# Optimization experiments

Hardware: AMD Instinct MI355X
Metric: run time of the kernel (lower is better)

The kernel has to match this reference:

```python
import jax, jax.numpy as jnp
import numpy as np

EMBED_DIM = 2048
NUM_HEADS = 16
HEAD_DIM = EMBED_DIM // NUM_HEADS
SCALES = [(1, 1, 1), (1, 2, 2), (1, 4, 4), (1, 6, 6), (1, 8, 8),
          (1, 12, 12), (1, 16, 16), (1, 20, 20), (1, 24, 24), (1, 32, 32)]
LENS = [t * h * w for (t, h, w) in SCALES]
SEQ_LEN = int(np.sum(LENS))  # 2521
BATCH = 2
MAX_SCALE_MUL = float(np.log(100.0))


def _block_causal_bias():
    # VAR-style: queries in scale-block i attend to all keys up to end of block i.
    cum = np.cumsum(LENS)
    q_end = np.repeat(cum, LENS)                      # [L] visible kv length per query
    visible = np.arange(SEQ_LEN)[None, :] < q_end[:, None]
    bias = np.where(visible, 0.0, -np.inf).astype(np.float32)
    return jnp.asarray(bias)[None, None]              # [1,1,L,L]


def setup_inputs() -> dict:
    key = jax.random.key(0)
    ks = jax.random.split(key, 8)
    C, H, hd, L, B = EMBED_DIM, NUM_HEADS, HEAD_DIM, SEQ_LEN, BATCH
    x = jax.random.normal(ks[0], (B, L, C), dtype=jnp.float32)
    W_qkv = jax.random.normal(ks[1], (3 * C, C), dtype=jnp.float32) * (1.0 / np.sqrt(C))
    q_bias = jnp.zeros((C,), jnp.float32)
    v_bias = jnp.zeros((C,), jnp.float32)
    scale_mul_log = jnp.full((1, H, 1, 1), np.log(4.0), jnp.float32)
    proj_W = jax.random.normal(ks[2], (C, C), dtype=jnp.float32) * (1.0 / np.sqrt(C))
    proj_b = jnp.zeros((C,), jnp.float32)
    # 2D RoPE cache, pre-sliced for scale_ind=0: (2,1,1,1,L,hd//2) = (cos, sin)
    angles = jax.random.uniform(ks[3], (L, hd // 2), dtype=jnp.float32, maxval=2.0 * np.pi)
    rope_cache = jnp.stack([jnp.cos(angles), jnp.sin(angles)])[:, None, None, None]
    attn_bias = _block_causal_bias()
    return {"x": x, "W_qkv": W_qkv, "q_bias": q_bias, "v_bias": v_bias,
            "scale_mul_log": scale_mul_log, "proj_W": proj_W, "proj_b": proj_b,
            "rope_cache": rope_cache, "attn_bias": attn_bias}


def _l2norm(t, eps=1e-12):
    # torch F.normalize: x / max(||x||_2, eps)
    n = jnp.sqrt(jnp.sum(t * t, axis=-1, keepdims=True))
    return t / jnp.maximum(n, eps)


def reference(x, W_qkv, q_bias, v_bias, scale_mul_log, proj_W, proj_b, rope_cache, attn_bias):
    B, L, C = x.shape
    H, hd = NUM_HEADS, HEAD_DIM
    bias = jnp.concatenate([q_bias, jnp.zeros_like(q_bias), v_bias])
    qkv = x @ W_qkv.T + bias                               # [B,L,3C]
    qkv = qkv.reshape(B, L, 3, H, hd).transpose(2, 0, 3, 1, 4)  # [3,B,H,L,hd]
    q, k, v = qkv[0], qkv[1], qkv[2]
    # cosine attention: L2-norm q,k; q scaled by clamped learnable per-head scale
    scale_mul = jnp.exp(jnp.minimum(scale_mul_log, MAX_SCALE_MUL))
    q = _l2norm(q) * scale_mul
    k = _l2norm(k)
    # 2D RoPE applied jointly to q and k
    qk = jnp.stack([q, k]).reshape(2, B, H, L, hd // 2, 2)
    cos, sin = rope_cache[0], rope_cache[1]                # [1,1,1,L,hd//2]
    re = cos * qk[..., 0] - sin * qk[..., 1]
    im = sin * qk[..., 0] + cos * qk[..., 1]
    qk = jnp.stack([re, im], axis=-1).reshape(2, B, H, L, hd)
    q, k = qk[0], qk[1]
    # SDPA with scale=1 (cos_attn) and additive block-causal bias
    scores = jnp.einsum('bhqd,bhkd->bhqk', q, k) + attn_bias
    attn = jax.nn.softmax(scores, axis=-1)
    out = jnp.einsum('bhqk,bhkd->bhqd', attn, v)           # [B,H,L,hd]
    out = out.transpose(0, 2, 1, 3).reshape(B, L, C)
    return out @ proj_W.T + proj_b
```

## Files before the change

kernel.cpp:

```cpp
#include <hip/hip_runtime.h>
#include <stdint.h>

#define SEQL 2521
#define LPAD 2560
#define NB 2
#define NH 16
#define HD 128
#define CD 2048
#define KD 2048

typedef float f32x4 __attribute__((ext_vector_type(4)));
typedef __bf16 bf16x8 __attribute__((ext_vector_type(8)));
typedef unsigned short u16x8 __attribute__((ext_vector_type(8)));

static __device__ __forceinline__ unsigned short bf16r(float f){
  union { float f; unsigned u; } v; v.f = f;
  unsigned r = v.u + 0x7FFFu + ((v.u >> 16) & 1u);
  return (unsigned short)(r >> 16);
}
static __device__ __forceinline__ float bf2f(unsigned short s){
  union { unsigned u; float f; } v; v.u = ((unsigned)s) << 16; return v.f;
}
static __device__ __forceinline__ bf16x8 asbf(u16x8 v){ return __builtin_bit_cast(bf16x8, v); }

typedef const __attribute__((address_space(1))) unsigned int* gas1_t;
typedef __attribute__((address_space(3))) unsigned int* las3_t;
static __device__ __forceinline__ void glds16(const void* g, void* l){
  __builtin_amdgcn_global_load_lds((gas1_t)g, (las3_t)l, 16, 0, 0);
}

__global__ __launch_bounds__(256) void prep_kernel(
    const float* __restrict__ x, const float* __restrict__ wqkv, const float* __restrict__ projw,
    unsigned short* __restrict__ xb, unsigned short* __restrict__ wb, unsigned short* __restrict__ pw)
{
  const int NX = (NB*LPAD*CD)/4;
  const int NW = (3*CD*CD)/4;
  const int NPj = (CD*CD)/4;
  const int total = NX + NW + NPj;
  for (int v = blockIdx.x*256 + threadIdx.x; v < total; v += gridDim.x*256){
    if (v < NX){
      int e = v << 2;
      int row = e >> 11, col = e & 2047;
      int b = (row >= LPAD) ? 1 : 0;
      int l = row - b*LPAD;
      ushort4 o;
      if (l < SEQL){
        const float4 f = *(const float4*)(x + (((long)(b*SEQL + l)) << 11) + col);
        o.x = bf16r(f.x); o.y = bf16r(f.y); o.z = bf16r(f.z); o.w = bf16r(f.w);
      } else { o.x = 0; o.y = 0; o.z = 0; o.w = 0; }
      *(ushort4*)(xb + e) = o;
    } else if (v < NX + NW){
      long i = (long)(v - NX) << 2;
      const float4 f = *(const float4*)(wqkv + i);
      ushort4 o; o.x=bf16r(f.x); o.y=bf16r(f.y); o.z=bf16r(f.z); o.w=bf16r(f.w);
      *(ushort4*)(wb + i) = o;
    } else {
      long i = (long)(v - NX - NW) << 2;
      const float4 f = *(const float4*)(projw + i);
      ushort4 o; o.x=bf16r(f.x); o.y=bf16r(f.y); o.z=bf16r(f.z); o.w=bf16r(f.w);
      *(ushort4*)(pw + i) = o;
    }
  }
}

static __device__ __forceinline__ void gemm_core(
    const unsigned short* __restrict__ A, const unsigned short* __restrict__ Bm,
    unsigned short* As, unsigned short* Bs, int m0, int n0, f32x4 acc[4][4])
{
  const int tid = threadIdx.x;
  const int w = tid >> 6, lane = tid & 63;
  const int g = lane >> 4, lr = lane & 15;
  const int wm = w >> 1, wn = w & 1;
  const unsigned short* aS0 = A + (long)(m0 + (tid >> 2))*KD + ((tid & 3) << 3);
  const unsigned short* aS1 = aS0 + (long)64*KD;
  const unsigned short* bS0 = Bm + (long)(n0 + (tid >> 2))*KD + ((tid & 3) << 3);
  const unsigned short* bS1 = bS0 + (long)64*KD;
  unsigned short* aD0 = As + (w << 9);
  unsigned short* aD1 = As + 2048 + (w << 9);
  unsigned short* bD0 = Bs + (w << 9);
  unsigned short* bD1 = Bs + 2048 + (w << 9);
  const unsigned short* aRd = As + ((wm << 6) + lr)*32 + (g << 3);
  const unsigned short* bRd = Bs + ((wn << 6) + lr)*32 + (g << 3);
  for (int kt = 0; kt < KD/32; ++kt){
    __syncthreads();
    const int ko = kt << 5;
    glds16(aS0 + ko, aD0);
    glds16(aS1 + ko, aD1);
    glds16(bS0 + ko, bD0);
    glds16(bS1 + ko, bD1);
    __syncthreads();
    u16x8 af[4], bfr[4];
#pragma unroll
    for (int i = 0; i < 4; ++i) af[i]  = *(const u16x8*)(aRd + i*16*32);
#pragma unroll
    for (int j = 0; j < 4; ++j) bfr[j] = *(const u16x8*)(bRd + j*16*32);
#pragma unroll
    for (int i = 0; i < 4; ++i)
#pragma unroll
      for (int j = 0; j < 4; ++j)
        acc[i][j] = __builtin_amdgcn_mfma_f32_16x16x32_bf16(asbf(af[i]), asbf(bfr[j]), acc[i][j], 0, 0, 0);
  }
}

__global__ __launch_bounds__(256) void gemm_qkv(
    const unsigned short* __restrict__ A, const unsigned short* __restrict__ W,
    const float* __restrict__ qb, const float* __restrict__ vb,
    unsigned short* __restrict__ qg, unsigned short* __restrict__ kg,
    unsigned short* __restrict__ vt)
{
  __shared__ __align__(16) unsigned short As[128*32];
  __shared__ __align__(16) unsigned short Bs[128*32];
  f32x4 acc[4][4] = {};
  const int m0 = blockIdx.x << 7, n0 = blockIdx.y << 7;
  gemm_core(A, W, As, Bs, m0, n0, acc);
  const int tid = threadIdx.x;
  const int w = tid >> 6, lane = tid & 63, g = lane >> 4, lr = lane & 15;
  const int wm = w >> 1, wn = w & 1;
  const int part = n0 >> 11;
  const int b = (m0 >= LPAD) ? 1 : 0;
  const int l0 = m0 - b*LPAD;
  const int hb = (n0 & 2047) >> 7;
#pragma unroll
  for (int ai = 0; ai < 4; ++ai){
#pragma unroll
    for (int bj = 0; bj < 4; ++bj){
      const int d = (wn << 6) + (bj << 4) + lr;
      const int mloc = (wm << 6) + (ai << 4) + (g << 2);
      const float bias = (part == 0) ? qb[(hb << 7) + d] : ((part == 2) ? vb[(hb << 7) + d] : 0.f);
      const f32x4 v = acc[ai][bj];
      if (part == 2){
        ushort4 o;
        o.x = bf16r(v[0] + bias); o.y = bf16r(v[1] + bias);
        o.z = bf16r(v[2] + bias); o.w = bf16r(v[3] + bias);
        *(ushort4*)(vt + ((long)((b*NH + hb)*HD + d))*LPAD + l0 + mloc) = o;
      } else {
        unsigned short* dst = (part ? kg : qg) + (((long)(b*NH + hb)*LPAD) + l0 + mloc)*HD + d;
        dst[0]     = bf16r(v[0] + bias);
        dst[HD]    = bf16r(v[1] + bias);
        dst[2*HD]  = bf16r(v[2] + bias);
        dst[3*HD]  = bf16r(v[3] + bias);
      }
    }
  }
}

__global__ __launch_bounds__(256) void gemm_proj(
    const unsigned short* __restrict__ A, const unsigned short* __restrict__ W,
    const float* __restrict__ pbias, float* __restrict__ out)
{
  __shared__ __align__(16) unsigned short As[128*32];
  __shared__ __align__(16) unsigned short Bs[128*32];
  f32x4 acc[4][4] = {};
  const int m0 = blockIdx.x << 7, n0 = blockIdx.y << 7;
  gemm_core(A, W, As, Bs, m0, n0, acc);
  const int tid = threadIdx.x;
  const int w = tid >> 6, lane = tid & 63, g = lane >> 4, lr = lane & 15;
  const int wm = w >> 1, wn = w & 1;
  const int b = (m0 >= LPAD) ? 1 : 0;
  const int l0 = m0 - b*LPAD;
#pragma unroll
  for (int ai = 0; ai < 4; ++ai){
#pragma unroll
    for (int bj = 0; bj < 4; ++bj){
      const int n = n0 + (wn << 6) + (bj << 4) + lr;
      const int mloc = (wm << 6) + (ai << 4) + (g << 2);
      const float bias = pbias[n];
      const f32x4 v = acc[ai][bj];
#pragma unroll
      for (int r = 0; r < 4; ++r){
        const int l = l0 + mloc + r;
        if (l < SEQL) out[(((long)b*SEQL + l) << 11) + n] = v[r] + bias;
      }
    }
  }
}

__global__ __launch_bounds__(256) void rope_norm(
    unsigned short* __restrict__ qg, unsigned short* __restrict__ kg,
    const float* __restrict__ rope, const float* __restrict__ smlog)
{
  const int w = threadIdx.x >> 6, lane = threadIdx.x & 63;
  const int l = blockIdx.x*4 + w;
  if (l >= SEQL) return;
  const int pb = blockIdx.y;
  const int part = pb >> 5, bh = pb & 31, h = bh & 15;
  unsigned short* base = (part ? kg : qg) + ((long)bh*LPAD + l)*HD + (lane << 1);
  const unsigned u = *(const unsigned*)base;
  const float re = bf2f((unsigned short)(u & 0xffff));
  const float im = bf2f((unsigned short)(u >> 16));
  float ss = re*re + im*im;
#pragma unroll
  for (int o = 1; o < 64; o <<= 1) ss += __shfl_xor(ss, o, 64);
  float inv = 1.f / fmaxf(sqrtf(ss), 1e-12f);
  if (part == 0){
    float sl = smlog[h];
    sl = fminf(sl, 4.605170185988091f);
    inv *= __expf(sl);
  }
  const float cs = rope[l*64 + lane];
  const float sn = rope[SEQL*64 + l*64 + lane];
  const float re2 = (cs*re - sn*im)*inv;
  const float im2 = (sn*re + cs*im)*inv;
  const unsigned o = (unsigned)bf16r(re2) | ((unsigned)bf16r(im2) << 16);
  *(unsigned*)base = o;
}

static __device__ __forceinline__ int q_end_of(int q){
  if (q >= SEQL) return 1;
  if (q < 121){
    if (q < 1) return 1;
    if (q < 5) return 5;
    if (q < 21) return 21;
    if (q < 57) return 57;
    return 121;
  }
  if (q < 265) return 265;
  if (q < 521) return 521;
  if (q < 921) return 921;
  if (q < 1497) return 1497;
  return 2521;
}

__global__ __launch_bounds__(256) void attn_kernel(
    const unsigned short* __restrict__ qg, const unsigned short* __restrict__ kg,
    const unsigned short* __restrict__ vt, unsigned short* __restrict__ aout)
{
  __shared__ __align__(16) unsigned short Ks[64*128];
  __shared__ __align__(16) unsigned short Vs[128*64];
  __shared__ __align__(16) unsigned short Ps[4][16*72];
  const int tid = threadIdx.x, w = tid >> 6, lane = tid & 63;
  const int g = lane >> 4, lr = lane & 15;
  const int qt = blockIdx.x, bh = blockIdx.y;
  const int q0 = qt << 6, qw = q0 + (w << 4);
  const long kvBase = (long)bh * LPAD * HD;

  u16x8 qf[4];
  {
    const unsigned short* qrow = qg + kvBase + (long)(qw + lr)*HD + (g << 3);
#pragma unroll
    for (int c = 0; c < 4; ++c) qf[c] = *(const u16x8*)(qrow + (c << 5));
  }
  const int qe = q_end_of(qw + lr);
  const int qmax = (q0 + 63 < SEQL - 1) ? q0 + 63 : SEQL - 1;
  const int nt = (q_end_of(qmax) + 63) >> 6;

  float m_run = -1e30f, l_run = 0.f;
  f32x4 acco[8] = {};

  for (int t = 0; t < nt; ++t){
    __syncthreads();
    const int kvb = t << 6;
#pragma unroll
    for (int c = 0; c < 4; ++c){
      const int idx = (c << 8) + tid;
      const int kv = idx >> 4, ch = idx & 15;
      glds16(kg + kvBase + (long)(kvb + kv)*HD + ((ch ^ (kv & 7)) << 3),
             Ks + (c << 11) + (w << 9));
      const int dd = idx >> 3, ch2 = idx & 7;
      glds16(vt + kvBase + (long)dd*LPAD + kvb + ((ch2 ^ (dd & 7)) << 3),
             Vs + (c << 11) + (w << 9));
    }
    __syncthreads();

    f32x4 accs[4] = {};
#pragma unroll
    for (int mf = 0; mf < 4; ++mf){
      const int kvr = (mf << 4) + lr;
      const unsigned short* krow = Ks + kvr*HD;
      const int sw = kvr & 7;
#pragma unroll
      for (int c = 0; c < 4; ++c){
        u16x8 kf = *(const u16x8*)(krow + ((((c << 2) + g) ^ sw) << 3));
        accs[mf] = __builtin_amdgcn_mfma_f32_16x16x32_bf16(asbf(kf), asbf(qf[c]), accs[mf], 0, 0, 0);
      }
    }

    float tmax = -1e30f;
#pragma unroll
    for (int mf = 0; mf < 4; ++mf){
#pragma unroll
      for (int r = 0; r < 4; ++r){
        const int kvg = kvb + (mf << 4) + (g << 2) + r;
        float s = (kvg < qe) ? accs[mf][r] : -1e30f;
        accs[mf][r] = s;
        tmax = fmaxf(tmax, s);
      }
    }
    tmax = fmaxf(tmax, __shfl_xor(tmax, 16, 64));
    tmax = fmaxf(tmax, __shfl_xor(tmax, 32, 64));
    const float mnew = fmaxf(m_run, tmax);
    const float alpha = __expf(m_run - mnew);
    float tsum = 0.f;
#pragma unroll
    for (int mf = 0; mf < 4; ++mf){
#pragma unroll
      for (int r = 0; r < 4; ++r){
        const float p = __expf(accs[mf][r] - mnew);
        accs[mf][r] = p;
        tsum += p;
      }
    }
    tsum += __shfl_xor(tsum, 16, 64);
    tsum += __shfl_xor(tsum, 32, 64);
    l_run = l_run*alpha + tsum;
    m_run = mnew;

    const float a0 = __shfl(alpha, (g << 2) + 0, 64);
    const float a1 = __shfl(alpha, (g << 2) + 1, 64);
    const float a2 = __shfl(alpha, (g << 2) + 2, 64);
    const float a3 = __shfl(alpha, (g << 2) + 3, 64);
#pragma unroll
    for (int nf = 0; nf < 8; ++nf){
      acco[nf][0] *= a0; acco[nf][1] *= a1; acco[nf][2] *= a2; acco[nf][3] *= a3;
    }

    unsigned short* prow = &Ps[w][lr*72 + (g << 2)];
#pragma unroll
    for (int mf = 0; mf < 4; ++mf){
      uint2 pk;
      pk.x = (unsigned)bf16r(accs[mf][0]) | ((unsigned)bf16r(accs[mf][1]) << 16);
      pk.y = (unsigned)bf16r(accs[mf][2]) | ((unsigned)bf16r(accs[mf][3]) << 16);
      *(uint2*)(prow + (mf << 4)) = pk;
    }

#pragma unroll
    for (int c = 0; c < 2; ++c){
      u16x8 pf = *(const u16x8*)(&Ps[w][lr*72 + (c << 5) + (g << 3)]);
      const int sw2 = lr & 7;
#pragma unroll
      for (int nf = 0; nf < 8; ++nf){
        u16x8 vf = *(const u16x8*)(Vs + ((nf << 4) + lr)*64 + ((((c << 2) + g) ^ sw2) << 3));
        acco[nf] = __builtin_amdgcn_mfma_f32_16x16x32_bf16(asbf(pf), asbf(vf), acco[nf], 0, 0, 0);
      }
    }
  }

  const float rcp = 1.f / l_run;
  const float li0 = __shfl(rcp, (g << 2) + 0, 64);
  const float li1 = __shfl(rcp, (g << 2) + 1, 64);
  const float li2 = __shfl(rcp, (g << 2) + 2, 64);
  const float li3 = __shfl(rcp, (g << 2) + 3, 64);
  const int b = bh >> 4, h = bh & 15;
#pragma unroll
  for (int r = 0; r < 4; ++r){
    const int qq = qw + (g << 2) + r;
    if (qq < SEQL){
      const float lir = (r == 0) ? li0 : ((r == 1) ? li1 : ((r == 2) ? li2 : li3));
      unsigned short* dst = aout + (((long)(b*LPAD + qq)) << 11) + (h << 7) + lr;
#pragma unroll
      for (int nf = 0; nf < 8; ++nf)
        dst[nf << 4] = bf16r(acco[nf][r] * lir);
    }
  }
}

extern "C" void kernel_launch(void* const* d_in, const int* in_sizes, int n_in,
                              void* d_out, int out_size, void* d_ws, size_t ws_size,
                              hipStream_t stream) {
  const float* x     = (const float*)d_in[0];
  const float* wqkv  = (const float*)d_in[1];
  const float* qb    = (const float*)d_in[2];
  const float* vb    = (const float*)d_in[3];
  const float* smlog = (const float*)d_in[4];
  const float* projw = (const float*)d_in[5];
  const float* projb = (const float*)d_in[6];
  const float* rope  = (const float*)d_in[7];
  float* out = (float*)d_out;

  unsigned short* xb = (unsigned short*)d_ws;
  unsigned short* wb = xb + (size_t)NB*LPAD*CD;
  unsigned short* pw = wb + (size_t)3*CD*CD;
  unsigned short* qg = pw + (size_t)CD*CD;
  unsigned short* kg = qg + (size_t)NB*NH*LPAD*HD;
  unsigned short* vt = kg + (size_t)NB*NH*LPAD*HD;

  prep_kernel<<<2048, 256, 0, stream>>>(x, wqkv, projw, xb, wb, pw);
  gemm_qkv<<<dim3(40, 48), 256, 0, stream>>>(xb, wb, qb, vb, qg, kg, vt);
  rope_norm<<<dim3(631, 64), 256, 0, stream>>>(qg, kg, rope, smlog);
  attn_kernel<<<dim3(40, 32), 256, 0, stream>>>(qg, kg, vt, xb);
  gemm_proj<<<dim3(40, 16), 256, 0, stream>>>(xb, pw, projb, out);
}
```

Baseline: 610.6 us.

## Rework attention tiling, lazy softmax rescale, vectorized rope_norm and native bf16 casts

The attention kernel now uses 512 threads and 128-query tiles, so each K/V tile load is shared by 8 waves. Blocks launch heaviest-first, and full tiles skip the causal mask. The softmax works in base 2 (log2e folded into the q scale) and only rescales the accumulator when the running max rises by more than a threshold. MFMA sections are wrapped in s_setprio. rope_norm is vectorized to 16 lanes per row with 8-element loads, and the manual bf16 rounding is replaced by native casts. These changes target redundant K/V traffic, exp and rescale work, and shuffle overhead, at the cost of more LDS per block and fewer blocks in the grid.

```diff
diff --git a/kernel.cpp b/kernel.cpp
--- a/kernel.cpp
+++ b/kernel.cpp
@@ -13,10 +13,9 @@
 typedef __bf16 bf16x8 __attribute__((ext_vector_type(8)));
 typedef unsigned short u16x8 __attribute__((ext_vector_type(8)));
 
-static __device__ __forceinline__ unsigned short bf16r(float f){
-  union { float f; unsigned u; } v; v.f = f;
-  unsigned r = v.u + 0x7FFFu + ((v.u >> 16) & 1u);
-  return (unsigned short)(r >> 16);
+static __device__ __forceinline__ unsigned short bf16c(float f){
+  __bf16 h = (__bf16)f;
+  return __builtin_bit_cast(unsigned short, h);
 }
 static __device__ __forceinline__ float bf2f(unsigned short s){
   union { unsigned u; float f; } v; v.u = ((unsigned)s) << 16; return v.f;
@@ -46,18 +45,18 @@
       ushort4 o;
       if (l < SEQL){
         const float4 f = *(const float4*)(x + (((long)(b*SEQL + l)) << 11) + col);
-        o.x = bf16r(f.x); o.y = bf16r(f.y); o.z = bf16r(f.z); o.w = bf16r(f.w);
+        o.x = bf16c(f.x); o.y = bf16c(f.y); o.z = bf16c(f.z); o.w = bf16c(f.w);
       } else { o.x = 0; o.y = 0; o.z = 0; o.w = 0; }
       *(ushort4*)(xb + e) = o;
     } else if (v < NX + NW){
       long i = (long)(v - NX) << 2;
       const float4 f = *(const float4*)(wqkv + i);
-      ushort4 o; o.x=bf16r(f.x); o.y=bf16r(f.y); o.z=bf16r(f.z); o.w=bf16r(f.w);
+      ushort4 o; o.x=bf16c(f.x); o.y=bf16c(f.y); o.z=bf16c(f.z); o.w=bf16c(f.w);
       *(ushort4*)(wb + i) = o;
     } else {
       long i = (long)(v - NX - NW) << 2;
       const float4 f = *(const float4*)(projw + i);
-      ushort4 o; o.x=bf16r(f.x); o.y=bf16r(f.y); o.z=bf16r(f.z); o.w=bf16r(f.w);
+      ushort4 o; o.x=bf16c(f.x); o.y=bf16c(f.y); o.z=bf16c(f.z); o.w=bf16c(f.w);
       *(ushort4*)(pw + i) = o;
     }
   }
@@ -130,15 +129,15 @@
       const f32x4 v = acc[ai][bj];
       if (part == 2){
         ushort4 o;
-        o.x = bf16r(v[0] + bias); o.y = bf16r(v[1] + bias);
-        o.z = bf16r(v[2] + bias); o.w = bf16r(v[3] + bias);
+        o.x = bf16c(v[0] + bias); o.y = bf16c(v[1] + bias);
+        o.z = bf16c(v[2] + bias); o.w = bf16c(v[3] + bias);
         *(ushort4*)(vt + ((long)((b*NH + hb)*HD + d))*LPAD + l0 + mloc) = o;
       } else {
         unsigned short* dst = (part ? kg : qg) + (((long)(b*NH + hb)*LPAD) + l0 + mloc)*HD + d;
-        dst[0]     = bf16r(v[0] + bias);
-        dst[HD]    = bf16r(v[1] + bias);
-        dst[2*HD]  = bf16r(v[2] + bias);
-        dst[3*HD]  = bf16r(v[3] + bias);
+        dst[0]     = bf16c(v[0] + bias);
+        dst[HD]    = bf16c(v[1] + bias);
+        dst[2*HD]  = bf16c(v[2] + bias);
+        dst[3*HD]  = bf16c(v[3] + bias);
       }
     }
   }
@@ -179,30 +178,40 @@
     unsigned short* __restrict__ qg, unsigned short* __restrict__ kg,
     const float* __restrict__ rope, const float* __restrict__ smlog)
 {
-  const int w = threadIdx.x >> 6, lane = threadIdx.x & 63;
-  const int l = blockIdx.x*4 + w;
+  const int sub = threadIdx.x & 15;
+  const int l = blockIdx.x*16 + (threadIdx.x >> 4);
   if (l >= SEQL) return;
   const int pb = blockIdx.y;
   const int part = pb >> 5, bh = pb & 31, h = bh & 15;
-  unsigned short* base = (part ? kg : qg) + ((long)bh*LPAD + l)*HD + (lane << 1);
-  const unsigned u = *(const unsigned*)base;
-  const float re = bf2f((unsigned short)(u & 0xffff));
-  const float im = bf2f((unsigned short)(u >> 16));
-  float ss = re*re + im*im;
-#pragma unroll
-  for (int o = 1; o < 64; o <<= 1) ss += __shfl_xor(ss, o, 64);
+  unsigned short* base = (part ? kg : qg) + ((long)bh*LPAD + l)*HD + (sub << 3);
+  const u16x8 v = *(const u16x8*)base;
+  float f[8];
+#pragma unroll
+  for (int i = 0; i < 8; ++i) f[i] = bf2f(v[i]);
+  float ss = 0.f;
+#pragma unroll
+  for (int i = 0; i < 8; ++i) ss += f[i]*f[i];
+  ss += __shfl_xor(ss, 1, 16);
+  ss += __shfl_xor(ss, 2, 16);
+  ss += __shfl_xor(ss, 4, 16);
+  ss += __shfl_xor(ss, 8, 16);
   float inv = 1.f / fmaxf(sqrtf(ss), 1e-12f);
   if (part == 0){
-    float sl = smlog[h];
-    sl = fminf(sl, 4.605170185988091f);
-    inv *= __expf(sl);
-  }
-  const float cs = rope[l*64 + lane];
-  const float sn = rope[SEQL*64 + l*64 + lane];
-  const float re2 = (cs*re - sn*im)*inv;
-  const float im2 = (sn*re + cs*im)*inv;
-  const unsigned o = (unsigned)bf16r(re2) | ((unsigned)bf16r(im2) << 16);
-  *(unsigned*)base = o;
+    float sl = fminf(smlog[h], 4.605170185988091f);
+    inv *= __expf(sl) * 1.4426950408889634f;
+  }
+  const float4 cs = *(const float4*)(rope + (long)l*64 + (sub << 2));
+  const float4 sn = *(const float4*)(rope + (long)(SEQL + l)*64 + (sub << 2));
+  u16x8 o;
+  const float c4[4] = {cs.x, cs.y, cs.z, cs.w};
+  const float s4[4] = {sn.x, sn.y, sn.z, sn.w};
+#pragma unroll
+  for (int p = 0; p < 4; ++p){
+    const float re = f[2*p], im = f[2*p+1];
+    o[2*p]   = bf16c((c4[p]*re - s4[p]*im)*inv);
+    o[2*p+1] = bf16c((s4[p]*re + c4[p]*im)*inv);
+  }
+  *(u16x8*)base = o;
 }
 
 static __device__ __forceinline__ int q_end_of(int q){
@@ -221,17 +230,18 @@
   return 2521;
 }
 
-__global__ __launch_bounds__(256) void attn_kernel(
+__global__ __launch_bounds__(512) void attn_kernel(
     const unsigned short* __restrict__ qg, const unsigned short* __restrict__ kg,
     const unsigned short* __restrict__ vt, unsigned short* __restrict__ aout)
 {
   __shared__ __align__(16) unsigned short Ks[64*128];
   __shared__ __align__(16) unsigned short Vs[128*64];
-  __shared__ __align__(16) unsigned short Ps[4][16*72];
+  __shared__ __align__(16) unsigned short Ps[8][16*72];
   const int tid = threadIdx.x, w = tid >> 6, lane = tid & 63;
   const int g = lane >> 4, lr = lane & 15;
-  const int qt = blockIdx.x, bh = blockIdx.y;
-  const int q0 = qt << 6, qw = q0 + (w << 4);
+  const int qt = (int)gridDim.x - 1 - (int)blockIdx.x;
+  const int bh = blockIdx.y;
+  const int q0 = qt << 7, qw = q0 + (w << 4);
   const long kvBase = (long)bh * LPAD * HD;
 
   u16x8 qf[4];
@@ -240,29 +250,31 @@
 #pragma unroll
     for (int c = 0; c < 4; ++c) qf[c] = *(const u16x8*)(qrow + (c << 5));
   }
-  const int qe = q_end_of(qw + lr);
-  const int qmax = (q0 + 63 < SEQL - 1) ? q0 + 63 : SEQL - 1;
+  const int qe  = q_end_of(qw + lr);
+  const int qe0 = q_end_of(qw);
+  const int qmax = (q0 + 127 < SEQL - 1) ? q0 + 127 : SEQL - 1;
   const int nt = (q_end_of(qmax) + 63) >> 6;
 
-  float m_run = -1e30f, l_run = 0.f;
+  float m2 = -1e30f, l_run = 0.f;
   f32x4 acco[8] = {};
 
   for (int t = 0; t < nt; ++t){
     __syncthreads();
     const int kvb = t << 6;
 #pragma unroll
-    for (int c = 0; c < 4; ++c){
-      const int idx = (c << 8) + tid;
+    for (int c = 0; c < 2; ++c){
+      const int idx = (c << 9) + tid;
       const int kv = idx >> 4, ch = idx & 15;
       glds16(kg + kvBase + (long)(kvb + kv)*HD + ((ch ^ (kv & 7)) << 3),
-             Ks + (c << 11) + (w << 9));
+             Ks + (c << 12) + (w << 9));
       const int dd = idx >> 3, ch2 = idx & 7;
       glds16(vt + kvBase + (long)dd*LPAD + kvb + ((ch2 ^ (dd & 7)) << 3),
-             Vs + (c << 11) + (w << 9));
+             Vs + (c << 12) + (w << 9));
     }
     __syncthreads();
 
     f32x4 accs[4] = {};
+    __builtin_amdgcn_s_setprio(1);
 #pragma unroll
     for (int mf = 0; mf < 4; ++mf){
       const int kvr = (mf << 4) + lr;
@@ -274,28 +286,51 @@
         accs[mf] = __builtin_amdgcn_mfma_f32_16x16x32_bf16(asbf(kf), asbf(qf[c]), accs[mf], 0, 0, 0);
       }
     }
+    __builtin_amdgcn_s_setprio(0);
 
     float tmax = -1e30f;
-#pragma unroll
-    for (int mf = 0; mf < 4; ++mf){
-#pragma unroll
-      for (int r = 0; r < 4; ++r){
-        const int kvg = kvb + (mf << 4) + (g << 2) + r;
-        float s = (kvg < qe) ? accs[mf][r] : -1e30f;
-        accs[mf][r] = s;
-        tmax = fmaxf(tmax, s);
+    if (kvb + 64 <= qe0){
+#pragma unroll
+      for (int mf = 0; mf < 4; ++mf)
+#pragma unroll
+        for (int r = 0; r < 4; ++r) tmax = fmaxf(tmax, accs[mf][r]);
+    } else {
+#pragma unroll
+      for (int mf = 0; mf < 4; ++mf){
+#pragma unroll
+        for (int r = 0; r < 4; ++r){
+          const int kvg = kvb + (mf << 4) + (g << 2) + r;
+          float s = (kvg < qe) ? accs[mf][r] : -1e30f;
+          accs[mf][r] = s;
+          tmax = fmaxf(tmax, s);
+        }
       }
     }
     tmax = fmaxf(tmax, __shfl_xor(tmax, 16, 64));
     tmax = fmaxf(tmax, __shfl_xor(tmax, 32, 64));
-    const float mnew = fmaxf(m_run, tmax);
-    const float alpha = __expf(m_run - mnew);
+
+    float alpha = 1.f;
+    const bool need = !__all(tmax <= m2 + 11.0f);
+    if (need){
+      const float mnew = fmaxf(m2, tmax);
+      alpha = exp2f(m2 - mnew);
+      m2 = mnew;
+      const float a0 = __shfl(alpha, (g << 2) + 0, 64);
+      const float a1 = __shfl(alpha, (g << 2) + 1, 64);
+      const float a2 = __shfl(alpha, (g << 2) + 2, 64);
+      const float a3 = __shfl(alpha, (g << 2) + 3, 64);
+#pragma unroll
+      for (int nf = 0; nf < 8; ++nf){
+        acco[nf][0] *= a0; acco[nf][1] *= a1; acco[nf][2] *= a2; acco[nf][3] *= a3;
+      }
+    }
+
     float tsum = 0.f;
 #pragma unroll
     for (int mf = 0; mf < 4; ++mf){
 #pragma unroll
       for (int r = 0; r < 4; ++r){
-        const float p = __expf(accs[mf][r] - mnew);
+        const float p = exp2f(accs[mf][r] - m2);
         accs[mf][r] = p;
         tsum += p;
       }
@@ -303,26 +338,17 @@
     tsum += __shfl_xor(tsum, 16, 64);
     tsum += __shfl_xor(tsum, 32, 64);
     l_run = l_run*alpha + tsum;
-    m_run = mnew;
-
-    const float a0 = __shfl(alpha, (g << 2) + 0, 64);
-    const float a1 = __shfl(alpha, (g << 2) + 1, 64);
-    const float a2 = __shfl(alpha, (g << 2) + 2, 64);
-    const float a3 = __shfl(alpha, (g << 2) + 3, 64);
-#pragma unroll
-    for (int nf = 0; nf < 8; ++nf){
-      acco[nf][0] *= a0; acco[nf][1] *= a1; acco[nf][2] *= a2; acco[nf][3] *= a3;
-    }
 
     unsigned short* prow = &Ps[w][lr*72 + (g << 2)];
 #pragma unroll
     for (int mf = 0; mf < 4; ++mf){
       uint2 pk;
-      pk.x = (unsigned)bf16r(accs[mf][0]) | ((unsigned)bf16r(accs[mf][1]) << 16);
-      pk.y = (unsigned)bf16r(accs[mf][2]) | ((unsigned)bf16r(accs[mf][3]) << 16);
+      pk.x = (unsigned)bf16c(accs[mf][0]) | ((unsigned)bf16c(accs[mf][1]) << 16);
+      pk.y = (unsigned)bf16c(accs[mf][2]) | ((unsigned)bf16c(accs[mf][3]) << 16);
       *(uint2*)(prow + (mf << 4)) = pk;
     }
 
+    __builtin_amdgcn_s_setprio(1);
 #pragma unroll
     for (int c = 0; c < 2; ++c){
       u16x8 pf = *(const u16x8*)(&Ps[w][lr*72 + (c << 5) + (g << 3)]);
@@ -333,6 +359,7 @@
         acco[nf] = __builtin_amdgcn_mfma_f32_16x16x32_bf16(asbf(pf), asbf(vf), acco[nf], 0, 0, 0);
       }
     }
+    __builtin_amdgcn_s_setprio(0);
   }
 
   const float rcp = 1.f / l_run;
@@ -349,7 +376,7 @@
       unsigned short* dst = aout + (((long)(b*LPAD + qq)) << 11) + (h << 7) + lr;
 #pragma unroll
       for (int nf = 0; nf < 8; ++nf)
-        dst[nf << 4] = bf16r(acco[nf][r] * lir);
+        dst[nf << 4] = bf16c(acco[nf][r] * lir);
     }
   }
 }
@@ -376,7 +403,7 @@
 
   prep_kernel<<<2048, 256, 0, stream>>>(x, wqkv, projw, xb, wb, pw);
   gemm_qkv<<<dim3(40, 48), 256, 0, stream>>>(xb, wb, qb, vb, qg, kg, vt);
-  rope_norm<<<dim3(631, 64), 256, 0, stream>>>(qg, kg, rope, smlog);
-  attn_kernel<<<dim3(40, 32), 256, 0, stream>>>(qg, kg, vt, xb);
+  rope_norm<<<dim3(158, 64), 256, 0, stream>>>(qg, kg, rope, smlog);
+  attn_kernel<<<dim3(20, 32), 512, 0, stream>>>(qg, kg, vt, xb);
   gemm_proj<<<dim3(40, 16), 256, 0, stream>>>(xb, pw, projb, out);
 }
```

Measured after the change: 574.2 us. -6.0%, faster.
